# Optimization experiments

Hardware: AMD Instinct MI355X
Metric: run time of the kernel (lower is better)

The kernel has to match this reference:

```python
import jax, jax.numpy as jnp
import numpy as np

SIGMA = 0.5   # pairwise density bandwidth (density_std)
EPS = 1e-8
B, N, K, P, D, F, H = 8, 20, 2, 320, 3, 64, 64


def setup_inputs() -> dict:
    key = jax.random.key(0)
    ks = jax.random.split(key, 8)
    # ring graph: neighbor node index for each of the K=2 incident slots
    nbr = np.stack([(np.arange(N) - 1) % N, (np.arange(N) + 1) % N], axis=1).astype(np.int32)
    return {
        "X": jax.random.uniform(ks[0], (B, N, K, P, D), minval=-1.0, maxval=1.0),
        "W": jax.random.uniform(ks[1], (B, N, K, P), minval=0.1, maxval=1.0),
        "feats": jax.random.normal(ks[2], (B, N, F)),
        "mu": 0.1 * jax.random.normal(ks[3], (N, K, D)),
        "W1": jax.random.normal(ks[4], (N, F, H)) / np.sqrt(F),
        "Wx": jax.random.normal(ks[5], (N, D, H)) / np.sqrt(D),
        "b1": jnp.zeros((N, H), jnp.float32),
        "W2": jax.random.normal(ks[6], (N, H)) / np.sqrt(H),
        "bias2": jnp.zeros((N,), jnp.float32),
        "nbr_idx": jnp.asarray(nbr),
    }


def reference(X, W, feats, mu, W1, Wx, b1, W2, bias2, nbr_idx):
    # X: [B,N,K,P,D] belief/message particles, W: [B,N,K,P] particle weights
    Bs, Ns, Ks, Ps, Ds = X.shape
    KP = Ks * Ps
    # normalize incoming message weights per node (as in uniform_init: sum over K*P == 1)
    Wn = W / (W.sum(axis=(2, 3), keepdims=True) + EPS)
    Xf = X.reshape(Bs, Ns, KP, Ds)
    Wf = Wn.reshape(Bs, Ns, KP)
    # irregular gather of each node's neighbors' particles/weights
    Xn = Xf[:, nbr_idx]   # [B,N,K,KP,D]
    Wnb = Wf[:, nbr_idx]  # [B,N,K,KP]
    # pairwise edge density: Gaussian on (x_dst - mu_e) vs x_src, via ||a||^2+||b||^2-2ab
    a = X - mu[None, :, :, None, :]                      # [B,N,K,P,D]
    cross = jnp.einsum('bnkpd,bnkqd->bnkpq', a, Xn)      # [B,N,K,P,KP]
    d2 = (a * a).sum(-1)[..., None] + (Xn * Xn).sum(-1)[..., None, :] - 2.0 * cross
    kern = jnp.exp(-d2 / (2.0 * SIGMA * SIGMA))
    # neighbor message: weighted density sum over neighbor particles
    msg = jnp.einsum('bnkpq,bnkq->bnkp', kern, Wnb)      # [B,N,K,P]
    # per-node unary likelihood MLP on (image features, particle state)
    hf = jnp.einsum('bnf,nfh->bnh', feats, W1)           # [B,N,H]
    hx = jnp.einsum('bnkpd,ndh->bnkph', X, Wx)           # [B,N,K,P,H]
    h = jax.nn.relu(hf[:, :, None, None, :] + hx + b1[None, :, None, None, :])
    u = jax.nn.sigmoid(jnp.einsum('bnkph,nh->bnkp', h, W2) + bias2[None, :, None, None])
    # belief weight update: unary * neighbor message, renormalized per node
    w = u * msg
    return w / (w.sum(axis=(2, 3), keepdims=True) + EPS)
```

## Files before the change

### kernel.cpp

```cpp
#include <hip/hip_runtime.h>

constexpr int B_ = 8, N_ = 20, K_ = 2, P_ = 320, D_ = 3, F_ = 64, H_ = 64;
constexpr int Q_ = K_ * P_;
constexpr float EPS_ = 1e-8f;
constexpr float LOG2E_ = 1.4426950408889634f;
constexpr int TILES_ = 10;
constexpr int ROWS_  = 64;

__global__ __launch_bounds__(256) void main_kernel(
    const float* __restrict__ X,
    const float* __restrict__ W,
    const float* __restrict__ feats,
    const float* __restrict__ mu,
    const float* __restrict__ W1,
    const float* __restrict__ Wx,
    const float* __restrict__ b1,
    const float* __restrict__ W2,
    const float* __restrict__ bias2,
    const int* __restrict__ nbr,
    float* __restrict__ wsPart,
    float* __restrict__ out)
{
    __shared__ float4 sQ[Q_];
    __shared__ float4 aT[ROWS_];
    __shared__ float4 xT[ROWS_];
    __shared__ float4 gT[H_];
    __shared__ float  hbT[H_];
    __shared__ float  gpart[H_][5];
    __shared__ float  tgate[ROWS_][5];
    __shared__ float  part[ROWS_][17];
    __shared__ float  red[4];
    __shared__ float  invW;

    const int blk  = blockIdx.x;
    const int bn   = blk / TILES_;
    const int tile = blk - bn * TILES_;
    const int b    = bn / N_;
    const int n    = bn - b * N_;
    const int tid  = threadIdx.x;
    const int wave = tid >> 6;
    const int lane = tid & 63;
    const int k    = (tile >= 5) ? 1 : 0;
    const int r0   = tile * ROWS_;
    const int j    = nbr[n * 2 + k];

    const size_t nbase = ((size_t)b * N_ + j) * Q_;
    float wsum = 0.f;
    if (tid < Q_ / 4) {
        const int t = tid;
        const float4* xv = (const float4*)(X + nbase * D_);
        const float4 f0 = xv[3 * t];
        const float4 f1 = xv[3 * t + 1];
        const float4 f2 = xv[3 * t + 2];
        const float4 w4 = ((const float4*)(W + nbase))[t];
        const float c0 = w4.x * __builtin_amdgcn_exp2f(-2.f * LOG2E_ *
                         (f0.x * f0.x + f0.y * f0.y + f0.z * f0.z));
        const float c1 = w4.y * __builtin_amdgcn_exp2f(-2.f * LOG2E_ *
                         (f0.w * f0.w + f1.x * f1.x + f1.y * f1.y));
        const float c2 = w4.z * __builtin_amdgcn_exp2f(-2.f * LOG2E_ *
                         (f1.z * f1.z + f1.w * f1.w + f2.x * f2.x));
        const float c3 = w4.w * __builtin_amdgcn_exp2f(-2.f * LOG2E_ *
                         (f2.y * f2.y + f2.z * f2.z + f2.w * f2.w));
        sQ[4 * t]     = make_float4(f0.x, f0.y, f0.z, c0);
        sQ[4 * t + 1] = make_float4(f0.w, f1.x, f1.y, c1);
        sQ[4 * t + 2] = make_float4(f1.z, f1.w, f2.x, c2);
        sQ[4 * t + 3] = make_float4(f2.y, f2.z, f2.w, c3);
        wsum = (w4.x + w4.y) + (w4.z + w4.w);
    }
    {
        float v = wsum;
        #pragma unroll
        for (int off = 32; off > 0; off >>= 1) v += __shfl_down(v, off, 64);
        if (lane == 0) red[wave] = v;
    }

    {
        const int h = tid & 63, seg = tid >> 6;
        const float* fp  = feats + (size_t)bn * F_;
        const float* w1p = W1 + (size_t)n * F_ * H_ + h;
        float acc = 0.f;
        #pragma unroll
        for (int f = 0; f < 16; ++f) {
            const int ff = seg * 16 + f;
            acc = fmaf(fp[ff], w1p[(size_t)ff * H_], acc);
        }
        gpart[h][seg] = acc;
    }

    if (tid < ROWS_) {
        const int gr = r0 + tid;
        const float* xp = X + ((size_t)bn * Q_ + gr) * D_;
        const float x0 = xp[0], x1 = xp[1], x2 = xp[2];
        const float* mup = mu + (n * K_ + k) * D_;
        const float a0 = x0 - mup[0];
        const float a1 = x1 - mup[1];
        const float a2 = x2 - mup[2];
        const float ra2 = a0 * a0 + a1 * a1 + a2 * a2;
        aT[tid] = make_float4(a0 * (4.f * LOG2E_), a1 * (4.f * LOG2E_),
                              a2 * (4.f * LOG2E_), -2.f * LOG2E_ * ra2);
        xT[tid] = make_float4(x0, x1, x2, 0.f);
        const float* wxp = Wx + (size_t)n * D_ * H_ + tid;
        gT[tid] = make_float4(wxp[0], wxp[H_], wxp[2 * H_], W2[n * H_ + tid]);
    }
    __syncthreads();

    if (tid < H_)
        hbT[tid] = ((gpart[tid][0] + gpart[tid][1]) +
                    (gpart[tid][2] + gpart[tid][3])) + b1[n * H_ + tid];
    if (tid == 0)
        invW = 1.f / (((red[0] + red[1]) + (red[2] + red[3])) + EPS_);

    const int g = tid >> 4;
    const int s = tid & 15;
    float S0[4], S1[4], S2[4], RA[4], acc[4];
    #pragma unroll
    for (int jj = 0; jj < 4; ++jj) {
        const float4 av = aT[g * 4 + jj];
        S0[jj] = av.x; S1[jj] = av.y; S2[jj] = av.z; RA[jj] = av.w;
        acc[jj] = 0.f;
    }
    #pragma unroll 4
    for (int i = 0; i < Q_ / 16; ++i) {
        const float4 Pq = sQ[i * 16 + s];
        #pragma unroll
        for (int jj = 0; jj < 4; ++jj) {
            const float d = fmaf(Pq.x, S0[jj],
                            fmaf(Pq.y, S1[jj],
                            fmaf(Pq.z, S2[jj], RA[jj])));
            acc[jj] = fmaf(Pq.w, __builtin_amdgcn_exp2f(d), acc[jj]);
        }
    }
    #pragma unroll
    for (int jj = 0; jj < 4; ++jj)
        part[g * 4 + jj][s] = acc[jj];

    __syncthreads();

    {
        const int row = tid & 63, seg = tid >> 6;
        const float4 xr = xT[row];
        float accg = 0.f;
        #pragma unroll
        for (int hh = 0; hh < 16; ++hh) {
            const int h = seg * 16 + hh;
            const float4 gv = gT[h];
            float t = fmaf(xr.x, gv.x, fmaf(xr.y, gv.y, fmaf(xr.z, gv.z, hbT[h])));
            t = fmaxf(t, 0.f);
            accg = fmaf(t, gv.w, accg);
        }
        tgate[row][seg] = accg;
    }
    __syncthreads();

    if (tid < ROWS_) {
        const int row = tid;
        const float* pr = part[row];
        const float msg =
            (((pr[0] + pr[1]) + (pr[2] + pr[3])) + ((pr[4] + pr[5]) + (pr[6] + pr[7]))) +
            (((pr[8] + pr[9]) + (pr[10] + pr[11])) + ((pr[12] + pr[13]) + (pr[14] + pr[15])));
        const float accg = bias2[n] + ((tgate[row][0] + tgate[row][1]) +
                                       (tgate[row][2] + tgate[row][3]));
        const float u = 1.f / (1.f + __expf(-accg));
        const float wval = u * msg * invW;

        out[(size_t)bn * Q_ + r0 + row] = wval;

        float v = wval;
        #pragma unroll
        for (int off = 32; off > 0; off >>= 1) v += __shfl_down(v, off, 64);
        if (tid == 0) wsPart[blk] = v;
    }
}

__global__ __launch_bounds__(Q_) void norm_kernel(
    const float* __restrict__ wsPart, float* __restrict__ out)
{
    const int bn = blockIdx.x;
    const float* p = wsPart + bn * TILES_;
    float s0 = 0.f, s1 = 0.f;
    #pragma unroll
    for (int t = 0; t < TILES_ / 2; ++t) { s0 += p[2 * t]; s1 += p[2 * t + 1]; }
    const float inv = 1.f / ((s0 + s1) + EPS_);
    out[(size_t)bn * Q_ + threadIdx.x] *= inv;
}

extern "C" void kernel_launch(void* const* d_in, const int* in_sizes, int n_in,
                              void* d_out, int out_size, void* d_ws, size_t ws_size,
                              hipStream_t stream) {
    const float* X     = (const float*)d_in[0];
    const float* W     = (const float*)d_in[1];
    const float* feats = (const float*)d_in[2];
    const float* mu    = (const float*)d_in[3];
    const float* W1    = (const float*)d_in[4];
    const float* Wx    = (const float*)d_in[5];
    const float* b1    = (const float*)d_in[6];
    const float* W2    = (const float*)d_in[7];
    const float* bias2 = (const float*)d_in[8];
    const int*   nbr   = (const int*)d_in[9];
    float*       out   = (float*)d_out;
    float*       wsPart = (float*)d_ws;

    main_kernel<<<B_ * N_ * TILES_, 256, 0, stream>>>(
        X, W, feats, mu, W1, Wx, b1, W2, bias2, nbr, wsPart, out);
    norm_kernel<<<B_ * N_, Q_, 0, stream>>>(wsPart, out);
}
```

Before: 88.71 us.

## Fuse normalization into main kernel via cooperative grid sync

Replaces the two-kernel sequence (main + norm) with a single cooperative kernel that computes per-tile partial sums, performs a grid-wide sync, then normalizes outputs in registers. Tiles change from 10x64 rows to 8x80 rows per node, so 1280 blocks must be co-resident (launch bounds hint 5 blocks/CU). This removes a second launch and the read-modify-write of the output, at the cost of grid-sync overhead and occupancy constraints; it falls back to the old path if cooperative launch fails.

```diff
diff --git a/kernel.cpp b/kernel.cpp
--- a/kernel.cpp
+++ b/kernel.cpp
@@ -1,13 +1,17 @@
 #include <hip/hip_runtime.h>
+#include <hip/hip_cooperative_groups.h>
+
+namespace cg = cooperative_groups;
 
 constexpr int B_ = 8, N_ = 20, K_ = 2, P_ = 320, D_ = 3, F_ = 64, H_ = 64;
 constexpr int Q_ = K_ * P_;
 constexpr float EPS_ = 1e-8f;
 constexpr float LOG2E_ = 1.4426950408889634f;
-constexpr int TILES_ = 10;
-constexpr int ROWS_  = 64;
-
-__global__ __launch_bounds__(256) void main_kernel(
+
+constexpr int CT_ = 8;
+constexpr int CR_ = 80;
+
+__global__ __launch_bounds__(256, 5) void dnbp_coop(
     const float* __restrict__ X,
     const float* __restrict__ W,
     const float* __restrict__ feats,
@@ -22,26 +26,26 @@
     float* __restrict__ out)
 {
     __shared__ float4 sQ[Q_];
-    __shared__ float4 aT[ROWS_];
-    __shared__ float4 xT[ROWS_];
+    __shared__ float4 aT[CR_];
+    __shared__ float4 xT[CR_];
     __shared__ float4 gT[H_];
     __shared__ float  hbT[H_];
     __shared__ float  gpart[H_][5];
-    __shared__ float  tgate[ROWS_][5];
-    __shared__ float  part[ROWS_][17];
+    __shared__ float  tgate[CR_][5];
+    __shared__ float  part[CR_][17];
     __shared__ float  red[4];
     __shared__ float  invW;
 
     const int blk  = blockIdx.x;
-    const int bn   = blk / TILES_;
-    const int tile = blk - bn * TILES_;
+    const int bn   = blk >> 3;
+    const int tile = blk & 7;
     const int b    = bn / N_;
     const int n    = bn - b * N_;
     const int tid  = threadIdx.x;
     const int wave = tid >> 6;
     const int lane = tid & 63;
-    const int k    = (tile >= 5) ? 1 : 0;
-    const int r0   = tile * ROWS_;
+    const int k    = (tile >= 4) ? 1 : 0;
+    const int r0   = tile * CR_;
     const int j    = nbr[n * 2 + k];
 
     const size_t nbase = ((size_t)b * N_ + j) * Q_;
@@ -87,6 +91,195 @@
         gpart[h][seg] = acc;
     }
 
+    if (tid < CR_) {
+        const int gr = r0 + tid;
+        const float* xp = X + ((size_t)bn * Q_ + gr) * D_;
+        const float x0 = xp[0], x1 = xp[1], x2 = xp[2];
+        const float* mup = mu + (n * K_ + k) * D_;
+        const float a0 = x0 - mup[0];
+        const float a1 = x1 - mup[1];
+        const float a2 = x2 - mup[2];
+        const float ra2 = a0 * a0 + a1 * a1 + a2 * a2;
+        aT[tid] = make_float4(a0 * (4.f * LOG2E_), a1 * (4.f * LOG2E_),
+                              a2 * (4.f * LOG2E_), -2.f * LOG2E_ * ra2);
+        xT[tid] = make_float4(x0, x1, x2, 0.f);
+    }
+    if (tid < H_) {
+        const float* wxp = Wx + (size_t)n * D_ * H_ + tid;
+        gT[tid] = make_float4(wxp[0], wxp[H_], wxp[2 * H_], W2[n * H_ + tid]);
+    }
+    __syncthreads();
+
+    if (tid < H_)
+        hbT[tid] = ((gpart[tid][0] + gpart[tid][1]) +
+                    (gpart[tid][2] + gpart[tid][3])) + b1[n * H_ + tid];
+    if (tid == 0)
+        invW = 1.f / (((red[0] + red[1]) + (red[2] + red[3])) + EPS_);
+
+    const int g = tid >> 4;
+    const int s = tid & 15;
+    float S0[5], S1[5], S2[5], RA[5], acc[5];
+    #pragma unroll
+    for (int jj = 0; jj < 5; ++jj) {
+        const float4 av = aT[g * 5 + jj];
+        S0[jj] = av.x; S1[jj] = av.y; S2[jj] = av.z; RA[jj] = av.w;
+        acc[jj] = 0.f;
+    }
+    #pragma unroll 4
+    for (int i = 0; i < Q_ / 16; ++i) {
+        const float4 Pq = sQ[i * 16 + s];
+        #pragma unroll
+        for (int jj = 0; jj < 5; ++jj) {
+            const float d = fmaf(Pq.x, S0[jj],
+                            fmaf(Pq.y, S1[jj],
+                            fmaf(Pq.z, S2[jj], RA[jj])));
+            acc[jj] = fmaf(Pq.w, __builtin_amdgcn_exp2f(d), acc[jj]);
+        }
+    }
+    #pragma unroll
+    for (int jj = 0; jj < 5; ++jj)
+        part[g * 5 + jj][s] = acc[jj];
+
+    __syncthreads();
+
+    {
+        const int row = tid & 63, seg = tid >> 6;
+        const float4 xr = xT[row];
+        float accg = 0.f;
+        #pragma unroll
+        for (int hh = 0; hh < 16; ++hh) {
+            const int h = seg * 16 + hh;
+            const float4 gv = gT[h];
+            float t = fmaf(xr.x, gv.x, fmaf(xr.y, gv.y, fmaf(xr.z, gv.z, hbT[h])));
+            t = fmaxf(t, 0.f);
+            accg = fmaf(t, gv.w, accg);
+        }
+        tgate[row][seg] = accg;
+    }
+    if (tid < 64) {
+        const int row = 64 + (tid & 15), seg = tid >> 4;
+        const float4 xr = xT[row];
+        float accg = 0.f;
+        #pragma unroll
+        for (int hh = 0; hh < 16; ++hh) {
+            const int h = seg * 16 + hh;
+            const float4 gv = gT[h];
+            float t = fmaf(xr.x, gv.x, fmaf(xr.y, gv.y, fmaf(xr.z, gv.z, hbT[h])));
+            t = fmaxf(t, 0.f);
+            accg = fmaf(t, gv.w, accg);
+        }
+        tgate[row][seg] = accg;
+    }
+    __syncthreads();
+
+    float wval = 0.f;
+    if (tid < CR_) {
+        const int row = tid;
+        const float* pr = part[row];
+        const float msg =
+            (((pr[0] + pr[1]) + (pr[2] + pr[3])) + ((pr[4] + pr[5]) + (pr[6] + pr[7]))) +
+            (((pr[8] + pr[9]) + (pr[10] + pr[11])) + ((pr[12] + pr[13]) + (pr[14] + pr[15])));
+        const float accg = bias2[n] + ((tgate[row][0] + tgate[row][1]) +
+                                       (tgate[row][2] + tgate[row][3]));
+        const float u = 1.f / (1.f + __expf(-accg));
+        wval = u * msg * invW;
+    }
+    {
+        float v = wval;
+        #pragma unroll
+        for (int off = 32; off > 0; off >>= 1) v += __shfl_down(v, off, 64);
+        if (lane == 0) red[wave] = v;
+        __syncthreads();
+        if (tid == 0)
+            wsPart[blk] = (red[0] + red[1]) + (red[2] + red[3]);
+    }
+
+    cg::this_grid().sync();
+
+    if (tid < CR_) {
+        const float* p = wsPart + bn * CT_;
+        const float ssum = ((p[0] + p[1]) + (p[2] + p[3])) +
+                           ((p[4] + p[5]) + (p[6] + p[7]));
+        const float inv = 1.f / (ssum + EPS_);
+        out[(size_t)bn * Q_ + r0 + tid] = wval * inv;
+    }
+}
+
+constexpr int TILES_ = 10;
+constexpr int ROWS_  = 64;
+
+__global__ __launch_bounds__(256) void main_kernel(
+    const float* __restrict__ X, const float* __restrict__ W,
+    const float* __restrict__ feats, const float* __restrict__ mu,
+    const float* __restrict__ W1, const float* __restrict__ Wx,
+    const float* __restrict__ b1, const float* __restrict__ W2,
+    const float* __restrict__ bias2, const int* __restrict__ nbr,
+    float* __restrict__ wsPart, float* __restrict__ out)
+{
+    __shared__ float4 sQ[Q_];
+    __shared__ float4 aT[ROWS_];
+    __shared__ float4 xT[ROWS_];
+    __shared__ float4 gT[H_];
+    __shared__ float  hbT[H_];
+    __shared__ float  gpart[H_][5];
+    __shared__ float  tgate[ROWS_][5];
+    __shared__ float  part[ROWS_][17];
+    __shared__ float  red[4];
+    __shared__ float  invW;
+
+    const int blk  = blockIdx.x;
+    const int bn   = blk / TILES_;
+    const int tile = blk - bn * TILES_;
+    const int b    = bn / N_;
+    const int n    = bn - b * N_;
+    const int tid  = threadIdx.x;
+    const int wave = tid >> 6;
+    const int lane = tid & 63;
+    const int k    = (tile >= 5) ? 1 : 0;
+    const int r0   = tile * ROWS_;
+    const int j    = nbr[n * 2 + k];
+
+    const size_t nbase = ((size_t)b * N_ + j) * Q_;
+    float wsum = 0.f;
+    if (tid < Q_ / 4) {
+        const int t = tid;
+        const float4* xv = (const float4*)(X + nbase * D_);
+        const float4 f0 = xv[3 * t];
+        const float4 f1 = xv[3 * t + 1];
+        const float4 f2 = xv[3 * t + 2];
+        const float4 w4 = ((const float4*)(W + nbase))[t];
+        const float c0 = w4.x * __builtin_amdgcn_exp2f(-2.f * LOG2E_ *
+                         (f0.x * f0.x + f0.y * f0.y + f0.z * f0.z));
+        const float c1 = w4.y * __builtin_amdgcn_exp2f(-2.f * LOG2E_ *
+                         (f0.w * f0.w + f1.x * f1.x + f1.y * f1.y));
+        const float c2 = w4.z * __builtin_amdgcn_exp2f(-2.f * LOG2E_ *
+                         (f1.z * f1.z + f1.w * f1.w + f2.x * f2.x));
+        const float c3 = w4.w * __builtin_amdgcn_exp2f(-2.f * LOG2E_ *
+                         (f2.y * f2.y + f2.z * f2.z + f2.w * f2.w));
+        sQ[4 * t]     = make_float4(f0.x, f0.y, f0.z, c0);
+        sQ[4 * t + 1] = make_float4(f0.w, f1.x, f1.y, c1);
+        sQ[4 * t + 2] = make_float4(f1.z, f1.w, f2.x, c2);
+        sQ[4 * t + 3] = make_float4(f2.y, f2.z, f2.w, c3);
+        wsum = (w4.x + w4.y) + (w4.z + w4.w);
+    }
+    {
+        float v = wsum;
+        #pragma unroll
+        for (int off = 32; off > 0; off >>= 1) v += __shfl_down(v, off, 64);
+        if (lane == 0) red[wave] = v;
+    }
+    {
+        const int h = tid & 63, seg = tid >> 6;
+        const float* fp  = feats + (size_t)bn * F_;
+        const float* w1p = W1 + (size_t)n * F_ * H_ + h;
+        float acc = 0.f;
+        #pragma unroll
+        for (int f = 0; f < 16; ++f) {
+            const int ff = seg * 16 + f;
+            acc = fmaf(fp[ff], w1p[(size_t)ff * H_], acc);
+        }
+        gpart[h][seg] = acc;
+    }
     if (tid < ROWS_) {
         const int gr = r0 + tid;
         const float* xp = X + ((size_t)bn * Q_ + gr) * D_;
@@ -162,9 +355,7 @@
                                        (tgate[row][2] + tgate[row][3]));
         const float u = 1.f / (1.f + __expf(-accg));
         const float wval = u * msg * invW;
-
         out[(size_t)bn * Q_ + r0 + row] = wval;
-
         float v = wval;
         #pragma unroll
         for (int off = 32; off > 0; off >>= 1) v += __shfl_down(v, off, 64);
@@ -200,7 +391,15 @@
     float*       out   = (float*)d_out;
     float*       wsPart = (float*)d_ws;
 
-    main_kernel<<<B_ * N_ * TILES_, 256, 0, stream>>>(
-        X, W, feats, mu, W1, Wx, b1, W2, bias2, nbr, wsPart, out);
-    norm_kernel<<<B_ * N_, Q_, 0, stream>>>(wsPart, out);
+    void* args[] = {(void*)&X, (void*)&W, (void*)&feats, (void*)&mu,
+                    (void*)&W1, (void*)&Wx, (void*)&b1, (void*)&W2,
+                    (void*)&bias2, (void*)&nbr, (void*)&wsPart, (void*)&out};
+    const hipError_t err = hipLaunchCooperativeKernel(
+        (const void*)dnbp_coop, dim3(B_ * N_ * CT_), dim3(256), args, 0, stream);
+
+    if (err != hipSuccess) {
+        main_kernel<<<B_ * N_ * TILES_, 256, 0, stream>>>(
+            X, W, feats, mu, W1, Wx, b1, W2, bias2, nbr, wsPart, out);
+        norm_kernel<<<B_ * N_, Q_, 0, stream>>>(wsPart, out);
+    }
 }
```

Result: slower. 176.7 us (+99.2%).

## Fuse normalization into main kernel via last-block atomic counter, 80-row tiles

Applied to the files above, without the earlier changes.

Replaces the separate normalization kernel with a last-block-done pattern: each block writes unnormalized weights and a partial sum to workspace, increments a per-node atomic counter, and the final block normalizes the whole node. Tiles change from 10x64 rows to 8x80 rows so each thread handles 5 rows in the pairwise kernel loop, cutting the block count and the redundant neighbor staging per block. A small zero-counter kernel is added, so the launch count stays the same, and the final block does a serial extra pass over the node.

```diff
diff --git a/kernel.cpp b/kernel.cpp
--- a/kernel.cpp
+++ b/kernel.cpp
@@ -4,8 +4,18 @@
 constexpr int Q_ = K_ * P_;
 constexpr float EPS_ = 1e-8f;
 constexpr float LOG2E_ = 1.4426950408889634f;
-constexpr int TILES_ = 10;
-constexpr int ROWS_  = 64;
+constexpr int CT_ = 8;
+constexpr int CR_ = 80;
+
+constexpr size_t WV_OFF   = 0;
+constexpr size_t PART_OFF = (size_t)160 * Q_;
+constexpr size_t CNT_OFF  = PART_OFF + 1280;
+
+__global__ void zero_counters(int* __restrict__ cnt)
+{
+    const int i = threadIdx.x;
+    if (i < B_ * N_) cnt[i] = 0;
+}
 
 __global__ __launch_bounds__(256) void main_kernel(
     const float* __restrict__ X,
@@ -18,30 +28,33 @@
     const float* __restrict__ W2,
     const float* __restrict__ bias2,
     const int* __restrict__ nbr,
+    float* __restrict__ wsWv,
     float* __restrict__ wsPart,
+    int*   __restrict__ wsCnt,
     float* __restrict__ out)
 {
     __shared__ float4 sQ[Q_];
-    __shared__ float4 aT[ROWS_];
-    __shared__ float4 xT[ROWS_];
+    __shared__ float4 aT[CR_];
+    __shared__ float4 xT[CR_];
     __shared__ float4 gT[H_];
     __shared__ float  hbT[H_];
     __shared__ float  gpart[H_][5];
-    __shared__ float  tgate[ROWS_][5];
-    __shared__ float  part[ROWS_][17];
+    __shared__ float  tgate[CR_][5];
+    __shared__ float  part[CR_][17];
     __shared__ float  red[4];
     __shared__ float  invW;
+    __shared__ int    isLast;
 
     const int blk  = blockIdx.x;
-    const int bn   = blk / TILES_;
-    const int tile = blk - bn * TILES_;
+    const int bn   = blk >> 3;
+    const int tile = blk & 7;
     const int b    = bn / N_;
     const int n    = bn - b * N_;
     const int tid  = threadIdx.x;
     const int wave = tid >> 6;
     const int lane = tid & 63;
-    const int k    = (tile >= 5) ? 1 : 0;
-    const int r0   = tile * ROWS_;
+    const int k    = (tile >= 4) ? 1 : 0;
+    const int r0   = tile * CR_;
     const int j    = nbr[n * 2 + k];
 
     const size_t nbase = ((size_t)b * N_ + j) * Q_;
@@ -87,7 +100,7 @@
         gpart[h][seg] = acc;
     }
 
-    if (tid < ROWS_) {
+    if (tid < CR_) {
         const int gr = r0 + tid;
         const float* xp = X + ((size_t)bn * Q_ + gr) * D_;
         const float x0 = xp[0], x1 = xp[1], x2 = xp[2];
@@ -99,6 +112,8 @@
         aT[tid] = make_float4(a0 * (4.f * LOG2E_), a1 * (4.f * LOG2E_),
                               a2 * (4.f * LOG2E_), -2.f * LOG2E_ * ra2);
         xT[tid] = make_float4(x0, x1, x2, 0.f);
+    }
+    if (tid < H_) {
         const float* wxp = Wx + (size_t)n * D_ * H_ + tid;
         gT[tid] = make_float4(wxp[0], wxp[H_], wxp[2 * H_], W2[n * H_ + tid]);
     }
@@ -112,10 +127,10 @@
 
     const int g = tid >> 4;
     const int s = tid & 15;
-    float S0[4], S1[4], S2[4], RA[4], acc[4];
+    float S0[5], S1[5], S2[5], RA[5], acc[5];
     #pragma unroll
-    for (int jj = 0; jj < 4; ++jj) {
-        const float4 av = aT[g * 4 + jj];
+    for (int jj = 0; jj < 5; ++jj) {
+        const float4 av = aT[g * 5 + jj];
         S0[jj] = av.x; S1[jj] = av.y; S2[jj] = av.z; RA[jj] = av.w;
         acc[jj] = 0.f;
     }
@@ -123,7 +138,7 @@
     for (int i = 0; i < Q_ / 16; ++i) {
         const float4 Pq = sQ[i * 16 + s];
         #pragma unroll
-        for (int jj = 0; jj < 4; ++jj) {
+        for (int jj = 0; jj < 5; ++jj) {
             const float d = fmaf(Pq.x, S0[jj],
                             fmaf(Pq.y, S1[jj],
                             fmaf(Pq.z, S2[jj], RA[jj])));
@@ -131,8 +146,8 @@
         }
     }
     #pragma unroll
-    for (int jj = 0; jj < 4; ++jj)
-        part[g * 4 + jj][s] = acc[jj];
+    for (int jj = 0; jj < 5; ++jj)
+        part[g * 5 + jj][s] = acc[jj];
 
     __syncthreads();
 
@@ -150,9 +165,24 @@
         }
         tgate[row][seg] = accg;
     }
-    __syncthreads();
-
-    if (tid < ROWS_) {
+    if (tid < 64) {
+        const int row = 64 + (tid & 15), seg = tid >> 4;
+        const float4 xr = xT[row];
+        float accg = 0.f;
+        #pragma unroll
+        for (int hh = 0; hh < 16; ++hh) {
+            const int h = seg * 16 + hh;
+            const float4 gv = gT[h];
+            float t = fmaf(xr.x, gv.x, fmaf(xr.y, gv.y, fmaf(xr.z, gv.z, hbT[h])));
+            t = fmaxf(t, 0.f);
+            accg = fmaf(t, gv.w, accg);
+        }
+        tgate[row][seg] = accg;
+    }
+    __syncthreads();
+
+    float wval = 0.f;
+    if (tid < CR_) {
         const int row = tid;
         const float* pr = part[row];
         const float msg =
@@ -161,27 +191,38 @@
         const float accg = bias2[n] + ((tgate[row][0] + tgate[row][1]) +
                                        (tgate[row][2] + tgate[row][3]));
         const float u = 1.f / (1.f + __expf(-accg));
-        const float wval = u * msg * invW;
-
-        out[(size_t)bn * Q_ + r0 + row] = wval;
-
+        wval = u * msg * invW;
+        wsWv[(size_t)bn * Q_ + r0 + row] = wval;
+    }
+    {
         float v = wval;
         #pragma unroll
         for (int off = 32; off > 0; off >>= 1) v += __shfl_down(v, off, 64);
-        if (tid == 0) wsPart[blk] = v;
-    }
-}
-
-__global__ __launch_bounds__(Q_) void norm_kernel(
-    const float* __restrict__ wsPart, float* __restrict__ out)
-{
-    const int bn = blockIdx.x;
-    const float* p = wsPart + bn * TILES_;
-    float s0 = 0.f, s1 = 0.f;
-    #pragma unroll
-    for (int t = 0; t < TILES_ / 2; ++t) { s0 += p[2 * t]; s1 += p[2 * t + 1]; }
-    const float inv = 1.f / ((s0 + s1) + EPS_);
-    out[(size_t)bn * Q_ + threadIdx.x] *= inv;
+        if (lane == 0) red[wave] = v;
+        __syncthreads();
+        if (tid == 0)
+            wsPart[blk] = (red[0] + red[1]) + (red[2] + red[3]);
+    }
+
+    __threadfence();
+    __syncthreads();
+    if (tid == 0) {
+        const int old = __hip_atomic_fetch_add(&wsCnt[bn], 1, __ATOMIC_ACQ_REL,
+                                               __HIP_MEMORY_SCOPE_AGENT);
+        isLast = (old == CT_ - 1);
+    }
+    __syncthreads();
+    if (!isLast) return;
+    __threadfence();
+
+    const float* p = wsPart + bn * CT_;
+    const float ssum = ((p[0] + p[1]) + (p[2] + p[3])) +
+                       ((p[4] + p[5]) + (p[6] + p[7]));
+    const float inv = 1.f / (ssum + EPS_);
+    const float* wv = wsWv + (size_t)bn * Q_;
+    float* ob = out + (size_t)bn * Q_;
+    for (int r = tid; r < Q_; r += 256)
+        ob[r] = wv[r] * inv;
 }
 
 extern "C" void kernel_launch(void* const* d_in, const int* in_sizes, int n_in,
@@ -198,9 +239,13 @@
     const float* bias2 = (const float*)d_in[8];
     const int*   nbr   = (const int*)d_in[9];
     float*       out   = (float*)d_out;
-    float*       wsPart = (float*)d_ws;
-
-    main_kernel<<<B_ * N_ * TILES_, 256, 0, stream>>>(
-        X, W, feats, mu, W1, Wx, b1, W2, bias2, nbr, wsPart, out);
-    norm_kernel<<<B_ * N_, Q_, 0, stream>>>(wsPart, out);
+
+    float* wsf    = (float*)d_ws;
+    float* wsWv   = wsf + WV_OFF;
+    float* wsPart = wsf + PART_OFF;
+    int*   wsCnt  = (int*)(wsf + CNT_OFF);
+
+    zero_counters<<<1, 256, 0, stream>>>(wsCnt);
+    main_kernel<<<B_ * N_ * CT_, 256, 0, stream>>>(
+        X, W, feats, mu, W1, Wx, b1, W2, bias2, nbr, wsWv, wsPart, wsCnt, out);
 }
```

Result: slower. 206.9 us (+133.2%).
